# Optimization experiments

Measured on AMD Instinct MI355X. Metric: run time of the kernel, lower is better.

The kernel has to match this reference:

```python
import jax, jax.numpy as jnp
import numpy as np

N_NODES = 100_000
N_EDGES = 3_200_000
IN_DIM, HID_DIM, EMB_DIM = 128, 64, 32


def setup_inputs() -> dict:
    key = jax.random.key(0)
    k0, k1, k2, k3, k4, k5 = jax.random.split(key, 6)
    x = jax.random.normal(k0, (N_NODES, IN_DIM), dtype=jnp.float32)
    edge_index = jax.random.randint(k1, (2, N_EDGES), 0, N_NODES, dtype=jnp.int32)
    # GCNConv parameters (glorot-ish scale)
    W1 = jax.random.normal(k2, (IN_DIM, HID_DIM), dtype=jnp.float32) / np.sqrt(IN_DIM)
    b1 = jnp.zeros((HID_DIM,), dtype=jnp.float32)
    W2 = jax.random.normal(k3, (HID_DIM, EMB_DIM), dtype=jnp.float32) / np.sqrt(HID_DIM)
    b2 = jnp.zeros((EMB_DIM,), dtype=jnp.float32)
    return {"x": x, "W1": W1, "b1": b1, "W2": W2, "b2": b2, "edge_index": edge_index}


def reference(x, W1, b1, W2, b2, edge_index):
    """Two-layer GCN encoder (PyG GCNConv semantics, eval mode so dropout is a no-op).

    Each GCNConv: add self-loops, symmetric deg^-1/2 normalization,
    out = scatter_add(norm_e * (x @ W)[src], dst) + b.
    """
    N = x.shape[0]
    loops = jnp.arange(N, dtype=edge_index.dtype)
    src = jnp.concatenate([edge_index[0], loops])  # [E+N]
    dst = jnp.concatenate([edge_index[1], loops])  # [E+N]

    # degree of destination nodes (self-loops guarantee deg >= 1)
    deg = jax.ops.segment_sum(jnp.ones_like(dst, dtype=jnp.float32), dst,
                              num_segments=N)
    dinv = jax.lax.rsqrt(deg)                      # deg^-1/2, finite since deg>=1
    norm = dinv[src] * dinv[dst]                   # [E+N]

    def gcn_conv(h, W, b):
        h = h @ W                                  # dense transform [N, D_out]
        msg = h[src] * norm[:, None]               # gather + scale [E+N, D_out]
        return jax.ops.segment_sum(msg, dst, num_segments=N) + b

    h = jax.nn.relu(gcn_conv(x, W1, b1))
    # F.dropout with training=False is identity -> omitted
    return gcn_conv(h, W2, b2)
```

## Files before the change

### kernel.cpp

```cpp
#include <hip/hip_runtime.h>

static constexpr int NN = 100000;
static constexpr int NE = 3200000;
static constexpr int DI = 128;
static constexpr int DH = 64;
static constexpr int DO = 32;

static constexpr int NBK  = 391;
static constexpr int BCAP = 9216;
static constexpr int TILE = 4096;
static constexpr int NEB  = (NE + TILE - 1) / TILE;
static constexpr int NEBP = 784;
static constexpr int XW1_BASE = NEB + 1;
static constexpr int XW1_BLOCKS = (NN + 63) / 64;

typedef short short8 __attribute__((ext_vector_type(8)));
typedef float f32x4  __attribute__((ext_vector_type(4)));

__device__ __forceinline__ unsigned short f2bf(float f) {
    union { float f; unsigned u; } v; v.f = f;
    unsigned r = v.u + 0x7FFFu + ((v.u >> 16) & 1u);
    return (unsigned short)(r >> 16);
}
__device__ __forceinline__ float bflo(unsigned u) {
    union { unsigned u; float f; } v; v.u = u << 16; return v.f;
}
__device__ __forceinline__ float bfhi(unsigned u) {
    union { unsigned u; float f; } v; v.u = u & 0xFFFF0000u; return v.f;
}

__global__ __launch_bounds__(256) void k_count(
        const int* __restrict__ dst, int* __restrict__ cnt) {
    __shared__ int hist[NBK];
    int tid = threadIdx.x;
    for (int i = tid; i < NBK; i += 256) hist[i] = 0;
    __syncthreads();

    int base = blockIdx.x * TILE;
    int rem = NE - base;
#pragma unroll
    for (int k4 = 0; k4 < 4; ++k4) {
        int off = tid * 16 + k4 * 4;
        if (off < rem) {
            int4 d4 = *(const int4*)(dst + base + off);
            atomicAdd(&hist[(unsigned)d4.x >> 8], 1);
            atomicAdd(&hist[(unsigned)d4.y >> 8], 1);
            atomicAdd(&hist[(unsigned)d4.z >> 8], 1);
            atomicAdd(&hist[(unsigned)d4.w >> 8], 1);
        }
    }
    __syncthreads();
    for (int i = tid; i < NBK; i += 256)
        cnt[i * NEBP + blockIdx.x] = hist[i];
}

__global__ __launch_bounds__(64) void k_scan(
        int* __restrict__ cnt, int* __restrict__ bcur) {
    int b = blockIdx.x, tid = threadIdx.x;
    int* row = cnt + b * NEBP;
    int carry = 0;
    for (int c = 0; c < (NEB + 63) / 64; ++c) {
        int idx = c * 64 + tid;
        int v = (idx < NEB) ? row[idx] : 0;
        int inc = v;
#pragma unroll
        for (int o = 1; o < 64; o <<= 1) {
            int u = __shfl_up(inc, o, 64);
            if (tid >= o) inc += u;
        }
        int tot = __shfl(inc, 63, 64);
        if (idx < NEB) row[idx] = carry + inc - v;
        carry += tot;
    }
    if (tid == 0) bcur[b] = carry;
}

__global__ __launch_bounds__(256) void k_mega(
        const int* __restrict__ src, const int* __restrict__ dst,
        const int* __restrict__ gposM, int* __restrict__ bstore,
        const float* __restrict__ x, const float* __restrict__ W1,
        const float* __restrict__ W2,
        unsigned short* __restrict__ w2bf, unsigned short* __restrict__ h1b) {
    __shared__ int hist[NBK];
    __shared__ int lcur[NBK];
    __shared__ int gpos[NBK];
    __shared__ int stage[TILE];
    __shared__ unsigned short bid[TILE];

    int tid = threadIdx.x;

    if (blockIdx.x < NEB) {
        for (int i = tid; i < NBK; i += 256) hist[i] = 0;
        __syncthreads();

        int base = blockIdx.x * TILE;
        int rem = NE - base;
        int p[16]; unsigned short bb[16];
#pragma unroll
        for (int k4 = 0; k4 < 4; ++k4) {
            int off = tid * 16 + k4 * 4;
            if (off < rem) {
                int4 s4 = *(const int4*)(src + base + off);
                int4 d4 = *(const int4*)(dst + base + off);
                int k = 4 * k4;
                bb[k + 0] = (unsigned short)((unsigned)d4.x >> 8);
                p [k + 0] = ((d4.x & 255) << 24) | s4.x;
                atomicAdd(&hist[bb[k + 0]], 1);
                bb[k + 1] = (unsigned short)((unsigned)d4.y >> 8);
                p [k + 1] = ((d4.y & 255) << 24) | s4.y;
                atomicAdd(&hist[bb[k + 1]], 1);
                bb[k + 2] = (unsigned short)((unsigned)d4.z >> 8);
                p [k + 2] = ((d4.z & 255) << 24) | s4.z;
                atomicAdd(&hist[bb[k + 2]], 1);
                bb[k + 3] = (unsigned short)((unsigned)d4.w >> 8);
                p [k + 3] = ((d4.w & 255) << 24) | s4.w;
                atomicAdd(&hist[bb[k + 3]], 1);
            } else {
                int k = 4 * k4;
                bb[k + 0] = 0xFFFF; bb[k + 1] = 0xFFFF;
                bb[k + 2] = 0xFFFF; bb[k + 3] = 0xFFFF;
            }
        }
        __syncthreads();

        for (int i = tid; i < NBK; i += 256)
            gpos[i] = gposM[i * NEBP + blockIdx.x];
        __syncthreads();

        if (tid < 64) {
            int carry = 0;
            for (int c = 0; c < (NBK + 63) / 64; ++c) {
                int idx = c * 64 + tid;
                int v = (idx < NBK) ? hist[idx] : 0;
                int inc = v;
#pragma unroll
                for (int o = 1; o < 64; o <<= 1) {
                    int u = __shfl_up(inc, o, 64);
                    if (tid >= o) inc += u;
                }
                int tot = __shfl(inc, 63, 64);
                if (idx < NBK) { int ex = carry + inc - v; hist[idx] = ex; lcur[idx] = ex; }
                carry += tot;
            }
        }
        __syncthreads();

#pragma unroll
        for (int k = 0; k < 16; ++k) {
            if (bb[k] != 0xFFFF) {
                int lp = atomicAdd(&lcur[bb[k]], 1);
                stage[lp] = p[k];
                bid[lp] = bb[k];
            }
        }
        __syncthreads();

        int tcnt = min(TILE, rem);
        for (int i = tid; i < tcnt; i += 256) {
            int b = bid[i];
            int off = gpos[b] + (i - hist[b]);
            if (off < BCAP) bstore[b * BCAP + off] = stage[i];
        }
    } else if (blockIdx.x == NEB) {
        for (int i = tid; i < DH * DO; i += 256) w2bf[i] = f2bf(W2[i]);
    } else {
        int wave = tid >> 6, lane = tid & 63;
        int q = lane >> 4, m = lane & 15, o0 = wave * 16;
        int nb = (blockIdx.x - XW1_BASE) * 64;

        short8 bfr[4];
#pragma unroll
        for (int kb = 0; kb < 4; ++kb)
#pragma unroll
            for (int j = 0; j < 8; ++j)
                bfr[kb][j] = (short)f2bf(W1[(kb * 32 + q * 8 + j) * DH + o0 + m]);

#pragma unroll
        for (int mt = 0; mt < 4; ++mt) {
            int row = min(nb + mt * 16 + m, NN - 1);
            const float* xr = x + (size_t)row * DI;
            f32x4 acc = {0.f, 0.f, 0.f, 0.f};
#pragma unroll
            for (int kb = 0; kb < 4; ++kb) {
                f32x4 u0 = *(const f32x4*)(xr + kb * 32 + q * 8);
                f32x4 u1 = *(const f32x4*)(xr + kb * 32 + q * 8 + 4);
                short8 a;
                a[0] = (short)f2bf(u0.x); a[1] = (short)f2bf(u0.y);
                a[2] = (short)f2bf(u0.z); a[3] = (short)f2bf(u0.w);
                a[4] = (short)f2bf(u1.x); a[5] = (short)f2bf(u1.y);
                a[6] = (short)f2bf(u1.z); a[7] = (short)f2bf(u1.w);
                acc = __builtin_amdgcn_mfma_f32_16x16x32_bf16(a, bfr[kb], acc, 0, 0, 0);
            }
#pragma unroll
            for (int r = 0; r < 4; ++r) {
                int n = nb + mt * 16 + q * 4 + r;
                if (n < NN) h1b[(size_t)n * DH + o0 + m] = f2bf(acc[r]);
            }
        }
    }
}

__global__ __launch_bounds__(512) void k_bsort(
        const int* __restrict__ bcur, int* __restrict__ bstore,
        int* __restrict__ rpb, int* __restrict__ rpe, float* __restrict__ dinv,
        unsigned* __restrict__ h1) {
    __shared__ int buf[BCAP];
    __shared__ int sorted[BCAP];
    __shared__ int hist[256], scan[256], cur[256];
    __shared__ float sdinv[256];

    int b = blockIdx.x, tid = threadIdx.x;
    int cnt = min(bcur[b], BCAP);
    int base = b * BCAP;
    for (int i = tid; i < cnt; i += 512) buf[i] = bstore[base + i];
    if (tid < 256) hist[tid] = 0;
    __syncthreads();
    for (int i = tid; i < cnt; i += 512)
        atomicAdd(&hist[((unsigned)buf[i]) >> 24], 1);
    __syncthreads();

    if (tid < 64) {
        int carry = 0;
        for (int c = 0; c < 4; ++c) {
            int idx = c * 64 + tid;
            int v = hist[idx];
            int inc = v;
#pragma unroll
            for (int o = 1; o < 64; o <<= 1) {
                int u = __shfl_up(inc, o, 64);
                if (tid >= o) inc += u;
            }
            int tot = __shfl(inc, 63, 64);
            scan[idx] = carry + inc - v;
            cur[idx]  = carry + inc - v;
            carry += tot;
        }
    }
    __syncthreads();

    if (tid < 256) {
        int n = b * 256 + tid;
        if (n < NN) {
            int beg = base + scan[tid];
            rpb[n] = beg;
            rpe[n] = beg + hist[tid];
            float dv = rsqrtf(1.0f + (float)hist[tid]);
            dinv[n] = dv;
            sdinv[tid] = dv;
        }
    }

    for (int i = tid; i < cnt; i += 512) {
        unsigned pv = (unsigned)buf[i];
        int pos = atomicAdd(&cur[pv >> 24], 1);
        sorted[pos] = (int)(pv & 0xFFFFFF);
    }
    __syncthreads();
    for (int i = tid; i < cnt; i += 512) bstore[base + i] = sorted[i];

    for (int i = tid; i < 2048; i += 512) {
        int r = i >> 3, n = b * 256 + r;
        if (n < NN) {
            float dv = sdinv[r];
            uint4* p = (uint4*)h1 + (size_t)b * 2048 + i;
            uint4 u = *p;
            u.x = (unsigned)f2bf(bflo(u.x) * dv) | ((unsigned)f2bf(bfhi(u.x) * dv) << 16);
            u.y = (unsigned)f2bf(bflo(u.y) * dv) | ((unsigned)f2bf(bfhi(u.y) * dv) << 16);
            u.z = (unsigned)f2bf(bflo(u.z) * dv) | ((unsigned)f2bf(bfhi(u.z) * dv) << 16);
            u.w = (unsigned)f2bf(bflo(u.w) * dv) | ((unsigned)f2bf(bfhi(u.w) * dv) << 16);
            *p = u;
        }
    }
}

__global__ __launch_bounds__(256) void k_gather64(
        const int* __restrict__ rpb, const int* __restrict__ rpe,
        const int* __restrict__ csr, const unsigned* __restrict__ h,
        const float* __restrict__ dinv, const float* __restrict__ b1,
        unsigned* __restrict__ tbf) {
    int wave = threadIdx.x >> 6, lane = threadIdx.x & 63;
    int q = lane >> 3, f8 = lane & 7;
    int n = blockIdx.x * 4 + wave;
    int beg = rpb[n], end = rpe[n];
    float dn = dinv[n];

    float s0 = 0.f, s1 = 0.f, s2 = 0.f, s3 = 0.f;
    float s4 = 0.f, s5 = 0.f, s6 = 0.f, s7 = 0.f;
    if (q == 0) {
        uint4 u = *(const uint4*)(h + (size_t)n * 32 + 4 * f8);
        s0 = bflo(u.x); s1 = bfhi(u.x); s2 = bflo(u.y); s3 = bfhi(u.y);
        s4 = bflo(u.z); s5 = bfhi(u.z); s6 = bflo(u.w); s7 = bfhi(u.w);
    }
#define ACC8(U)                                                         \
    s0 += bflo(U.x); s1 += bfhi(U.x); s2 += bflo(U.y); s3 += bfhi(U.y); \
    s4 += bflo(U.z); s5 += bfhi(U.z); s6 += bflo(U.w); s7 += bfhi(U.w);

    for (int c = beg; c < end; c += 64) {
        int cnt = min(64, end - c);
        int sidx = (lane < cnt) ? csr[c + lane] : 0;
        int j = 0;
        for (; j + 16 <= cnt; j += 16) {
            int sa = __shfl(sidx, j + q, 64);
            int sb = __shfl(sidx, j + 8 + q, 64);
            uint4 ua = *(const uint4*)(h + (size_t)sa * 32 + 4 * f8);
            uint4 ub = *(const uint4*)(h + (size_t)sb * 32 + 4 * f8);
            ACC8(ua) ACC8(ub)
        }
        for (; j + 8 <= cnt; j += 8) {
            int sa = __shfl(sidx, j + q, 64);
            uint4 ua = *(const uint4*)(h + (size_t)sa * 32 + 4 * f8);
            ACC8(ua)
        }
        for (; j < cnt; j += 8) {
            int slot = j + q;
            int s = __shfl(sidx, slot, 64);
            if (slot < cnt) {
                uint4 u = *(const uint4*)(h + (size_t)s * 32 + 4 * f8);
                ACC8(u)
            }
        }
    }
#undef ACC8

#define RED8(m)                                                         \
    s0 += __shfl_xor(s0, m, 64); s1 += __shfl_xor(s1, m, 64);           \
    s2 += __shfl_xor(s2, m, 64); s3 += __shfl_xor(s3, m, 64);           \
    s4 += __shfl_xor(s4, m, 64); s5 += __shfl_xor(s5, m, 64);           \
    s6 += __shfl_xor(s6, m, 64); s7 += __shfl_xor(s7, m, 64);
    RED8(8) RED8(16) RED8(32)
#undef RED8

    if (q == 0) {
        float4 bA = *(const float4*)(b1 + 8 * f8);
        float4 bB = *(const float4*)(b1 + 8 * f8 + 4);
        float t0 = fmaxf(fmaf(s0, dn, bA.x), 0.f);
        float t1 = fmaxf(fmaf(s1, dn, bA.y), 0.f);
        float t2 = fmaxf(fmaf(s2, dn, bA.z), 0.f);
        float t3 = fmaxf(fmaf(s3, dn, bA.w), 0.f);
        float t4 = fmaxf(fmaf(s4, dn, bB.x), 0.f);
        float t5 = fmaxf(fmaf(s5, dn, bB.y), 0.f);
        float t6 = fmaxf(fmaf(s6, dn, bB.z), 0.f);
        float t7 = fmaxf(fmaf(s7, dn, bB.w), 0.f);
        uint4 o;
        o.x = (unsigned)f2bf(t0) | ((unsigned)f2bf(t1) << 16);
        o.y = (unsigned)f2bf(t2) | ((unsigned)f2bf(t3) << 16);
        o.z = (unsigned)f2bf(t4) | ((unsigned)f2bf(t5) << 16);
        o.w = (unsigned)f2bf(t6) | ((unsigned)f2bf(t7) << 16);
        *(uint4*)(tbf + (size_t)n * 32 + 4 * f8) = o;
    }
}

__global__ __launch_bounds__(256) void k_l2_mfma(
        const unsigned short* __restrict__ tbf, const unsigned short* __restrict__ w2bf,
        const float* __restrict__ dinv, unsigned short* __restrict__ h2b) {
    int wave = threadIdx.x >> 6, lane = threadIdx.x & 63;
    int q = lane >> 4, m = lane & 15;
    int o0 = (wave & 1) * 16, mt = wave >> 1;
    int nb = blockIdx.x * 32;

    short8 bf[2];
#pragma unroll
    for (int kb = 0; kb < 2; ++kb)
#pragma unroll
        for (int j = 0; j < 8; ++j)
            bf[kb][j] = (short)w2bf[(kb * 32 + q * 8 + j) * DO + o0 + m];

    int row = nb + mt * 16 + m;
    f32x4 acc = {0.f, 0.f, 0.f, 0.f};
#pragma unroll
    for (int kb = 0; kb < 2; ++kb) {
        short8 a = *(const short8*)(tbf + (size_t)row * DH + kb * 32 + q * 8);
        acc = __builtin_amdgcn_mfma_f32_16x16x32_bf16(a, bf[kb], acc, 0, 0, 0);
    }
#pragma unroll
    for (int r = 0; r < 4; ++r) {
        int n = nb + mt * 16 + q * 4 + r;
        if (n < NN) h2b[(size_t)n * DO + o0 + m] = f2bf(acc[r] * dinv[n]);
    }
}

__global__ __launch_bounds__(256) void k_gather32(
        const int* __restrict__ rpb, const int* __restrict__ rpe,
        const int* __restrict__ csr, const unsigned* __restrict__ h,
        const float* __restrict__ dinv, const float* __restrict__ b2,
        float* __restrict__ out) {
    int wave = threadIdx.x >> 6, lane = threadIdx.x & 63;
    int q = lane >> 2, f4 = lane & 3;
    int n = blockIdx.x * 4 + wave;
    int beg = rpb[n], end = rpe[n];

    float s0 = 0.f, s1 = 0.f, s2 = 0.f, s3 = 0.f;
    float s4 = 0.f, s5 = 0.f, s6 = 0.f, s7 = 0.f;
    if (q == 0) {
        uint4 u = *(const uint4*)(h + (size_t)n * 16 + 4 * f4);
        s0 = bflo(u.x); s1 = bfhi(u.x); s2 = bflo(u.y); s3 = bfhi(u.y);
        s4 = bflo(u.z); s5 = bfhi(u.z); s6 = bflo(u.w); s7 = bfhi(u.w);
    }
#define ACC8(U)                                                         \
    s0 += bflo(U.x); s1 += bfhi(U.x); s2 += bflo(U.y); s3 += bfhi(U.y); \
    s4 += bflo(U.z); s5 += bfhi(U.z); s6 += bflo(U.w); s7 += bfhi(U.w);

    for (int c = beg; c < end; c += 64) {
        int cnt = min(64, end - c);
        int sidx = (lane < cnt) ? csr[c + lane] : 0;
        int j = 0;
        for (; j + 32 <= cnt; j += 32) {
            int sa = __shfl(sidx, j + q, 64);
            int sb = __shfl(sidx, j + 16 + q, 64);
            uint4 ua = *(const uint4*)(h + (size_t)sa * 16 + 4 * f4);
            uint4 ub = *(const uint4*)(h + (size_t)sb * 16 + 4 * f4);
            ACC8(ua) ACC8(ub)
        }
        for (; j + 16 <= cnt; j += 16) {
            int sa = __shfl(sidx, j + q, 64);
            uint4 ua = *(const uint4*)(h + (size_t)sa * 16 + 4 * f4);
            ACC8(ua)
        }
        for (; j < cnt; j += 16) {
            int slot = j + q;
            int s = __shfl(sidx, slot, 64);
            if (slot < cnt) {
                uint4 u = *(const uint4*)(h + (size_t)s * 16 + 4 * f4);
                ACC8(u)
            }
        }
    }
#undef ACC8

#define RED8(m)                                                         \
    s0 += __shfl_xor(s0, m, 64); s1 += __shfl_xor(s1, m, 64);           \
    s2 += __shfl_xor(s2, m, 64); s3 += __shfl_xor(s3, m, 64);           \
    s4 += __shfl_xor(s4, m, 64); s5 += __shfl_xor(s5, m, 64);           \
    s6 += __shfl_xor(s6, m, 64); s7 += __shfl_xor(s7, m, 64);
    RED8(4) RED8(8) RED8(16) RED8(32)
#undef RED8

    if (q == 0) {
        float dn = dinv[n];
        float4 bA = *(const float4*)(b2 + 8 * f4);
        float4 bB = *(const float4*)(b2 + 8 * f4 + 4);
        size_t o = (size_t)n * 32 + 8 * f4;
        float4 oA, oB;
        oA.x = fmaf(s0, dn, bA.x); oA.y = fmaf(s1, dn, bA.y);
        oA.z = fmaf(s2, dn, bA.z); oA.w = fmaf(s3, dn, bA.w);
        oB.x = fmaf(s4, dn, bB.x); oB.y = fmaf(s5, dn, bB.y);
        oB.z = fmaf(s6, dn, bB.z); oB.w = fmaf(s7, dn, bB.w);
        *(float4*)(out + o) = oA;
        *(float4*)(out + o + 4) = oB;
    }
}

extern "C" void kernel_launch(void* const* d_in, const int* in_sizes, int n_in,
                              void* d_out, int out_size, void* d_ws, size_t ws_size,
                              hipStream_t stream) {
    const float* x  = (const float*)d_in[0];
    const float* W1 = (const float*)d_in[1];
    const float* b1 = (const float*)d_in[2];
    const float* W2 = (const float*)d_in[3];
    const float* b2 = (const float*)d_in[4];
    const int* ei  = (const int*)d_in[5];
    const int* src = ei;
    const int* dst = ei + NE;
    float* out = (float*)d_out;

    float* ws    = (float*)d_ws;
    int*   rpb   = (int*)ws;
    int*   rpe   = (int*)(ws + 100352);
    float* dinv  = ws + 200704;
    int*   bcur  = (int*)(ws + 301056);
    int*   bstor = (int*)(ws + 301568);
    unsigned short* w2bf = (unsigned short*)(ws + 3905024);
    unsigned short* tbf  = (unsigned short*)(ws + 3906048);
    unsigned short* h1b  = (unsigned short*)(ws + 7106048);
    unsigned short* h2b  = h1b;
    int*   cntM  = (int*)tbf;

    k_count    <<<NEB, 256, 0, stream>>>(dst, cntM);
    k_scan     <<<NBK, 64, 0, stream>>>(cntM, bcur);
    k_mega     <<<XW1_BASE + XW1_BLOCKS, 256, 0, stream>>>(
                    src, dst, cntM, bstor, x, W1, W2, w2bf, h1b);
    k_bsort    <<<NBK, 512, 0, stream>>>(bcur, bstor, rpb, rpe, dinv,
                                         (unsigned*)h1b);

    k_gather64 <<<NN / 4, 256, 0, stream>>>(rpb, rpe, bstor, (const unsigned*)h1b,
                                            dinv, b1, (unsigned*)tbf);
    k_l2_mfma  <<<NN / 32, 256, 0, stream>>>(tbf, w2bf, dinv, h2b);
    k_gather32 <<<NN / 4, 256, 0, stream>>>(rpb, rpe, bstor, (const unsigned*)h2b,
                                            dinv, b2, out);
}
```

Baseline: 276.3 us.

## Scatter edges directly to global buckets, dropping the LDS staging sort

The per-tile edge bucketing no longer builds a local histogram, scans it and stages packed edges in LDS before a coalesced write. Each edge now takes a slot by atomically incrementing the block's global bucket cursor held in LDS and is written straight to the bucket store. The edge tile doubles from 4096 to 8192, which halves the number of count and scatter blocks. This removes two barriers, an LDS scan and the staging buffers, but the global writes become scattered rather than contiguous runs per bucket, so write coalescing may suffer.

```diff
diff --git a/kernel.cpp b/kernel.cpp
--- a/kernel.cpp
+++ b/kernel.cpp
@@ -8,9 +8,9 @@
 
 static constexpr int NBK  = 391;
 static constexpr int BCAP = 9216;
-static constexpr int TILE = 4096;
+static constexpr int TILE = 8192;
 static constexpr int NEB  = (NE + TILE - 1) / TILE;
-static constexpr int NEBP = 784;
+static constexpr int NEBP = 392;
 static constexpr int XW1_BASE = NEB + 1;
 static constexpr int XW1_BLOCKS = (NN + 63) / 64;
 
@@ -39,8 +39,8 @@
     int base = blockIdx.x * TILE;
     int rem = NE - base;
 #pragma unroll
-    for (int k4 = 0; k4 < 4; ++k4) {
-        int off = tid * 16 + k4 * 4;
+    for (int k4 = 0; k4 < 8; ++k4) {
+        int off = tid * 32 + k4 * 4;
         if (off < rem) {
             int4 d4 = *(const int4*)(dst + base + off);
             atomicAdd(&hist[(unsigned)d4.x >> 8], 1);
@@ -81,85 +81,36 @@
         const float* __restrict__ x, const float* __restrict__ W1,
         const float* __restrict__ W2,
         unsigned short* __restrict__ w2bf, unsigned short* __restrict__ h1b) {
-    __shared__ int hist[NBK];
     __shared__ int lcur[NBK];
-    __shared__ int gpos[NBK];
-    __shared__ int stage[TILE];
-    __shared__ unsigned short bid[TILE];
 
     int tid = threadIdx.x;
 
     if (blockIdx.x < NEB) {
-        for (int i = tid; i < NBK; i += 256) hist[i] = 0;
+        for (int i = tid; i < NBK; i += 256)
+            lcur[i] = gposM[i * NEBP + blockIdx.x];
         __syncthreads();
 
         int base = blockIdx.x * TILE;
         int rem = NE - base;
-        int p[16]; unsigned short bb[16];
-#pragma unroll
-        for (int k4 = 0; k4 < 4; ++k4) {
-            int off = tid * 16 + k4 * 4;
+#pragma unroll
+        for (int k4 = 0; k4 < 8; ++k4) {
+            int off = tid * 32 + k4 * 4;
             if (off < rem) {
                 int4 s4 = *(const int4*)(src + base + off);
                 int4 d4 = *(const int4*)(dst + base + off);
-                int k = 4 * k4;
-                bb[k + 0] = (unsigned short)((unsigned)d4.x >> 8);
-                p [k + 0] = ((d4.x & 255) << 24) | s4.x;
-                atomicAdd(&hist[bb[k + 0]], 1);
-                bb[k + 1] = (unsigned short)((unsigned)d4.y >> 8);
-                p [k + 1] = ((d4.y & 255) << 24) | s4.y;
-                atomicAdd(&hist[bb[k + 1]], 1);
-                bb[k + 2] = (unsigned short)((unsigned)d4.z >> 8);
-                p [k + 2] = ((d4.z & 255) << 24) | s4.z;
-                atomicAdd(&hist[bb[k + 2]], 1);
-                bb[k + 3] = (unsigned short)((unsigned)d4.w >> 8);
-                p [k + 3] = ((d4.w & 255) << 24) | s4.w;
-                atomicAdd(&hist[bb[k + 3]], 1);
-            } else {
-                int k = 4 * k4;
-                bb[k + 0] = 0xFFFF; bb[k + 1] = 0xFFFF;
-                bb[k + 2] = 0xFFFF; bb[k + 3] = 0xFFFF;
-            }
-        }
-        __syncthreads();
-
-        for (int i = tid; i < NBK; i += 256)
-            gpos[i] = gposM[i * NEBP + blockIdx.x];
-        __syncthreads();
-
-        if (tid < 64) {
-            int carry = 0;
-            for (int c = 0; c < (NBK + 63) / 64; ++c) {
-                int idx = c * 64 + tid;
-                int v = (idx < NBK) ? hist[idx] : 0;
-                int inc = v;
-#pragma unroll
-                for (int o = 1; o < 64; o <<= 1) {
-                    int u = __shfl_up(inc, o, 64);
-                    if (tid >= o) inc += u;
-                }
-                int tot = __shfl(inc, 63, 64);
-                if (idx < NBK) { int ex = carry + inc - v; hist[idx] = ex; lcur[idx] = ex; }
-                carry += tot;
-            }
-        }
-        __syncthreads();
-
-#pragma unroll
-        for (int k = 0; k < 16; ++k) {
-            if (bb[k] != 0xFFFF) {
-                int lp = atomicAdd(&lcur[bb[k]], 1);
-                stage[lp] = p[k];
-                bid[lp] = bb[k];
-            }
-        }
-        __syncthreads();
-
-        int tcnt = min(TILE, rem);
-        for (int i = tid; i < tcnt; i += 256) {
-            int b = bid[i];
-            int off = gpos[b] + (i - hist[b]);
-            if (off < BCAP) bstore[b * BCAP + off] = stage[i];
+                int b0 = (unsigned)d4.x >> 8, p0 = ((d4.x & 255) << 24) | s4.x;
+                int b1 = (unsigned)d4.y >> 8, p1 = ((d4.y & 255) << 24) | s4.y;
+                int b2 = (unsigned)d4.z >> 8, p2 = ((d4.z & 255) << 24) | s4.z;
+                int b3 = (unsigned)d4.w >> 8, p3 = ((d4.w & 255) << 24) | s4.w;
+                int o0 = atomicAdd(&lcur[b0], 1);
+                int o1 = atomicAdd(&lcur[b1], 1);
+                int o2 = atomicAdd(&lcur[b2], 1);
+                int o3 = atomicAdd(&lcur[b3], 1);
+                if (o0 < BCAP) bstore[b0 * BCAP + o0] = p0;
+                if (o1 < BCAP) bstore[b1 * BCAP + o1] = p1;
+                if (o2 < BCAP) bstore[b2 * BCAP + o2] = p2;
+                if (o3 < BCAP) bstore[b3 * BCAP + o3] = p3;
+            }
         }
     } else if (blockIdx.x == NEB) {
         for (int i = tid; i < DH * DO; i += 256) w2bf[i] = f2bf(W2[i]);
```

Result: slower. 309.6 us (+12.1%).
